# Optimization experiments

Hardware: AMD Instinct MI355X
Metric: run time of the kernel (lower is better)

## Reference

```python
import jax, jax.numpy as jnp
import numpy as np
from jax.ops import segment_sum, segment_max

N, E, F, H, G, P, C = 50000, 600000, 128, 128, 64, 32, 10
HEADS = 3
BN_EPS = 1e-5
COS_EPS = 1e-8


def setup_inputs() -> dict:
    key = jax.random.key(0)
    ks = jax.random.split(key, 32)
    rn = lambda k, shape, s: jax.random.normal(k, shape, jnp.float32) * s
    inp = {
        "x": jax.random.normal(ks[0], (N, F), jnp.float32),
        "edge_index": jax.random.randint(ks[1], (2, E), 0, N, jnp.int32),
        "batch": jnp.sort(jax.random.randint(ks[2], (N,), 0, G, jnp.int32)),
        # GCNConv
        "W1": rn(ks[3], (F, H), F ** -0.5), "b1": jnp.zeros((H,), jnp.float32),
        # SAGEConv (lin_l on aggregated neighbors, lin_r on root)
        "Wl": rn(ks[4], (H, H), H ** -0.5), "Wr": rn(ks[5], (H, H), H ** -0.5),
        "bs": jnp.zeros((H,), jnp.float32),
        # GATConv, heads=3, concat=False
        "Wg": rn(ks[6], (H, HEADS * H), H ** -0.5),
        "a_src": rn(ks[7], (HEADS, H), H ** -0.5),
        "a_dst": rn(ks[8], (HEADS, H), H ** -0.5),
        "bg": jnp.zeros((H,), jnp.float32),
        # prototype head / classifier / decoder
        "protos": jax.random.normal(ks[9], (P, H), jnp.float32),
        "Wc": rn(ks[10], (H, C), H ** -0.5), "bc": jnp.zeros((C,), jnp.float32),
        "Wd1": rn(ks[11], (H, 2 * H), H ** -0.5), "bd1": jnp.zeros((2 * H,), jnp.float32),
        "Wd2": rn(ks[12], (2 * H, F), (2 * H) ** -0.5), "bd2": jnp.zeros((F,), jnp.float32),
    }
    # BatchNorm (eval mode): gamma, beta, running mean/var for bn1..bn3
    for i in range(3):
        k0, k1, k2 = jax.random.split(ks[13 + i], 3)
        inp[f"g{i+1}"] = 1.0 + rn(k0, (H,), 0.05)
        inp[f"be{i+1}"] = rn(k1, (H,), 0.05)
        inp[f"m{i+1}"] = rn(k2, (H,), 0.1)
        inp[f"v{i+1}"] = jnp.ones((H,), jnp.float32)
    return inp


def _bn(x, g, b, m, v):
    return (x - m) * jax.lax.rsqrt(v + BN_EPS) * g + b


def _forward(x, edge_index, batch,
             W1, b1, g1, be1, m1, v1,
             Wl, Wr, bs, g2, be2, m2, v2,
             Wg, a_src, a_dst, bg, g3, be3, m3, v3,
             protos, Wc, bc, Wd1, bd1, Wd2, bd2):
    src, dst = edge_index[0], edge_index[1]
    ones_e = jnp.ones((src.shape[0],), x.dtype)

    # --- GCNConv: symmetric norm with self-loops ---
    h = x @ W1                                        # [N, H]
    deg = segment_sum(ones_e, dst, num_segments=N) + 1.0
    dinv = jax.lax.rsqrt(deg)
    coef = dinv[src] * dinv[dst]                      # [E]
    h1 = segment_sum(h[src] * coef[:, None], dst, num_segments=N)
    h1 = h1 + h * (dinv * dinv)[:, None] + b1         # self-loop term + bias
    h1 = jax.nn.elu(_bn(h1, g1, be1, m1, v1))         # dropout = identity (eval)

    # --- SAGEConv: mean aggregation (no self-loops) ---
    cnt = segment_sum(ones_e, dst, num_segments=N)
    mean_nb = segment_sum(h1[src], dst, num_segments=N) / jnp.maximum(cnt, 1.0)[:, None]
    h2 = mean_nb @ Wl + h1 @ Wr + bs
    h2 = jax.nn.elu(_bn(h2, g2, be2, m2, v2))

    # --- GATConv: heads=3, concat=False (mean), with self-loops ---
    hg = (h2 @ Wg).reshape(N, HEADS, H)               # [N, 3, H]
    al_src = jnp.einsum('nhf,hf->nh', hg, a_src)      # [N, 3]
    al_dst = jnp.einsum('nhf,hf->nh', hg, a_dst)
    loop = jnp.arange(N, dtype=src.dtype)
    s2 = jnp.concatenate([src, loop])
    d2 = jnp.concatenate([dst, loop])
    e = jax.nn.leaky_relu(al_src[s2] + al_dst[d2], 0.2)   # [E+N, 3]
    emax = segment_max(e, d2, num_segments=N)             # every node has a self-loop
    ex = jnp.exp(e - emax[d2])
    den = segment_sum(ex, d2, num_segments=N)
    alpha = ex / den[d2]                                  # [E+N, 3]
    h3 = segment_sum(hg[s2] * alpha[:, :, None], d2, num_segments=N)
    h3 = h3.mean(axis=1) + bg                             # concat=False -> head mean
    h3 = jax.nn.elu(_bn(h3, g3, be3, m3, v3))

    # --- global mean pool over graphs ---
    gcnt = segment_sum(jnp.ones((N,), x.dtype), batch, num_segments=G)
    pooled = segment_sum(h3, batch, num_segments=G) / jnp.maximum(gcnt, 1.0)[:, None]

    # --- prototype head: cosine sim -> softmax -> mix ---
    xn = pooled / jnp.maximum(jnp.linalg.norm(pooled, axis=-1, keepdims=True), COS_EPS)
    pn = protos / jnp.maximum(jnp.linalg.norm(protos, axis=-1, keepdims=True), COS_EPS)
    sims = xn @ pn.T                                      # [G, P]
    assignments = jax.nn.softmax(sims, axis=-1)
    proto_emb = assignments @ protos                      # [G, H]
    logits = proto_emb @ Wc + bc                          # [G, C]
    reconstructed = jax.nn.relu(pooled @ Wd1 + bd1) @ Wd2 + bd2   # [G, F]
    return logits, proto_emb, assignments, reconstructed


def reference(x, edge_index, batch,
              W1, b1, g1, be1, m1, v1,
              Wl, Wr, bs, g2, be2, m2, v2,
              Wg, a_src, a_dst, bg, g3, be3, m3, v3,
              protos, Wc, bc, Wd1, bd1, Wd2, bd2):
    return _forward(x, edge_index, batch,
                    W1, b1, g1, be1, m1, v1,
                    Wl, Wr, bs, g2, be2, m2, v2,
                    Wg, a_src, a_dst, bg, g3, be3, m3, v3,
                    protos, Wc, bc, Wd1, bd1, Wd2, bd2)
```

## Files before the change

### kernel.cpp

```cpp
#include <hip/hip_runtime.h>
#include <hip/hip_bf16.h>
#include <stdint.h>
#include <stddef.h>

#define N_ 50000
#define E_ 600000
#define F_ 128
#define H_ 128
#define G_ 64
#define P_ 32
#define C_ 10
#define NB_ 49

typedef __hip_bfloat16 bf16;
typedef __attribute__((ext_vector_type(8))) short short8;
typedef __attribute__((ext_vector_type(4))) float float4v;

__device__ __forceinline__ float us2f(unsigned short u){ return __uint_as_float(((unsigned int)u)<<16); }
__device__ __forceinline__ unsigned short f2us(float x){ bf16 h = __float2bfloat16(x); return *(unsigned short*)&h; }
__device__ __forceinline__ float blo(unsigned int u){ return __uint_as_float(u<<16); }
__device__ __forceinline__ float bhi(unsigned int u){ return __uint_as_float(u & 0xFFFF0000u); }
__device__ __forceinline__ unsigned int packbf(float lo, float hi){ return ((unsigned int)f2us(hi)<<16) | f2us(lo); }
__device__ __forceinline__ float eluf(float x){ return x>0.f ? x : __expf(x)-1.f; }
__device__ __forceinline__ float bnf(float x,float m,float v,float g,float b){ return (x-m)*rsqrtf(v+1e-5f)*g+b; }
__device__ __forceinline__ float lrelu(float x){ return x>0.f ? x : 0.2f*x; }
__device__ __forceinline__ float expc(float x){ return __expf(fminf(x, 50.f)); }
__device__ __forceinline__ void atomAddF(float* a, float v){ unsafeAtomicAdd(a, v); }

__global__ __launch_bounds__(256) void k_wprep(const float* __restrict__ W1, const float* __restrict__ Wl,
    const float* __restrict__ Wr, const float* __restrict__ Wg, unsigned short* __restrict__ WT){
  int idx = blockIdx.x*256 + threadIdx.x;
  if(idx >= 6*16384) return;
  int m    = idx >> 14;
  int tile = (idx >> 11) & 7;
  int kc   = (idx >> 9) & 3;
  int lane = (idx >> 3) & 63;
  int j    = idx & 7;
  int k = kc*32 + (lane>>4)*8 + j;
  int n = tile*16 + (lane&15);
  float v;
  if(m==0)      v = W1[k*128+n];
  else if(m==1) v = Wl[k*128+n];
  else if(m==2) v = Wr[k*128+n];
  else          v = Wg[k*384 + (m-3)*128 + n];
  WT[idx] = f2us(v);
}

__global__ __launch_bounds__(384) void k_vprep(const float* __restrict__ Wg, const float* __restrict__ a_src,
    const float* __restrict__ a_dst, float* __restrict__ vs3, float* __restrict__ vd3){
  int t = threadIdx.x;
  if(t >= 384) return;
  int h = t >> 7, f = t & 127;
  const float4* wr = (const float4*)(Wg + (size_t)f*384 + h*128);
  const float4* as = (const float4*)(a_src + h*128);
  const float4* ad = (const float4*)(a_dst + h*128);
  float s = 0.f, d = 0.f;
  #pragma unroll 8
  for(int j=0;j<32;j++){
    float4 wv = wr[j], av = as[j], dv = ad[j];
    s += wv.x*av.x + wv.y*av.y + wv.z*av.z + wv.w*av.w;
    d += wv.x*dv.x + wv.y*dv.y + wv.z*dv.z + wv.w*dv.w;
  }
  vs3[t] = s; vd3[t] = d;
}

__device__ __forceinline__ void load_Afrag_bf16(const bf16* A, int row, int lane, short8 af[4]){
  const unsigned short* ap = (const unsigned short*)A + (size_t)row*128 + (lane>>4)*8;
  #pragma unroll
  for(int kc=0;kc<4;kc++) af[kc] = *(const short8*)(ap + kc*32);
}
__device__ __forceinline__ void mfma_pass_g(const unsigned short* __restrict__ WB, const short8 af[4],
                                            int lane, float4v acc[8]){
  #pragma unroll
  for(int tile=0;tile<8;tile++){
    #pragma unroll
    for(int kc=0;kc<4;kc++){
      short8 bfv = *(const short8*)(WB + (((tile*4+kc)*64 + lane)<<3));
      acc[tile] = __builtin_amdgcn_mfma_f32_16x16x32_bf16(af[kc], bfv, acc[tile], 0, 0, 0);
    }
  }
}

__global__ __launch_bounds__(256) void k_mm_x(const float* __restrict__ X, const unsigned short* __restrict__ WTg,
                                              bf16* __restrict__ HB){
// ... 162 lines not shown
                                              int* __restrict__ row_ptr){
  int lane = threadIdx.x;
  int v = (lane < NB_) ? bsum[lane] : 0;
  int x = v;
  #pragma unroll
  for(int o=1;o<64;o<<=1){
    int y = __shfl_up(x, o, 64);
    if(lane >= o) x += y;
  }
  if(lane < NB_) boff[lane] = x - v;
  if(lane == 63) row_ptr[N_] = x;
}

__global__ __launch_bounds__(256) void k_scan3(int* __restrict__ row_ptr, const int* __restrict__ boff,
                                               int* __restrict__ tmp){
  int i = blockIdx.x*256 + threadIdx.x;
  if(i < N_){
    int r = row_ptr[i] + boff[i>>10];
    row_ptr[i] = r;
    tmp[i] = r;
  }
}

__global__ __launch_bounds__(256) void k_scatter(const int* __restrict__ src, const int* __restrict__ dst,
                                                 int* __restrict__ tmp, int* __restrict__ esrc){
  int e = blockIdx.x*256 + threadIdx.x;
  if(e < E_){
    int d = dst[e];
    int pos = atomicAdd(&tmp[d], 1);
    esrc[pos] = src[e];
  }
}

__global__ __launch_bounds__(256) void k_gcn_gather(const int* __restrict__ row_ptr, const int* __restrict__ esrc,
    const float* __restrict__ dinv, const bf16* __restrict__ HB,
    const float* __restrict__ b1, const float* __restrict__ g1, const float* __restrict__ be1,
    const float* __restrict__ m1, const float* __restrict__ v1, bf16* __restrict__ H1B){
  int n = blockIdx.x*4 + (threadIdx.x>>6);
  int lane = threadIdx.x & 63;
  if(n >= N_) return;
  int beg = row_ptr[n], end = row_ptr[n+1];
  float dn = dinv[n];
  float a0 = 0.f, a1 = 0.f;
  const unsigned short* hb = (const unsigned short*)HB;
  int e = beg;
  for(; e+3 < end; e += 4){
    int s0 = esrc[e], s1 = esrc[e+1], s2 = esrc[e+2], s3 = esrc[e+3];
    unsigned int hv0 = *(const unsigned int*)(hb + (size_t)s0*H_ + lane*2);
    unsigned int hv1 = *(const unsigned int*)(hb + (size_t)s1*H_ + lane*2);
    unsigned int hv2 = *(const unsigned int*)(hb + (size_t)s2*H_ + lane*2);
    unsigned int hv3 = *(const unsigned int*)(hb + (size_t)s3*H_ + lane*2);
    float c0 = dinv[s0]*dn, c1 = dinv[s1]*dn, c2 = dinv[s2]*dn, c3 = dinv[s3]*dn;
    a0 += c0*blo(hv0) + c1*blo(hv1) + c2*blo(hv2) + c3*blo(hv3);
    a1 += c0*bhi(hv0) + c1*bhi(hv1) + c2*bhi(hv2) + c3*bhi(hv3);
  }
  for(; e < end; e++){
    int s = esrc[e];
    float c = dinv[s]*dn;
    unsigned int hv = *(const unsigned int*)(hb + (size_t)s*H_ + lane*2);
    a0 += c*blo(hv);
    a1 += c*bhi(hv);
  }
  unsigned int hv = *(const unsigned int*)(hb + (size_t)n*H_ + lane*2);
  int f0 = lane*2, f1 = f0+1;
  float x0 = a0 + blo(hv)*dn*dn + b1[f0];
  float x1 = a1 + bhi(hv)*dn*dn + b1[f1];
  x0 = eluf(bnf(x0, m1[f0], v1[f0], g1[f0], be1[f0]));
  x1 = eluf(bnf(x1, m1[f1], v1[f1], g1[f1], be1[f1]));
  unsigned int o = ((unsigned int)f2us(x1)<<16) | f2us(x0);
  *(unsigned int*)((unsigned short*)H1B + (size_t)n*H_ + lane*2) = o;
}

__global__ __launch_bounds__(256) void k_sage_gather(const int* __restrict__ row_ptr, const int* __restrict__ esrc,
    const bf16* __restrict__ H1B, bf16* __restrict__ MeanB){
  int n = blockIdx.x*4 + (threadIdx.x>>6);
  int lane = threadIdx.x & 63;
  if(n >= N_) return;
  int beg = row_ptr[n], end = row_ptr[n+1];
  float a0 = 0.f, a1 = 0.f;
  const unsigned short* hb = (const unsigned short*)H1B;
  int e = beg;
  for(; e+3 < end; e += 4){
    int s0 = esrc[e], s1 = esrc[e+1], s2 = esrc[e+2], s3 = esrc[e+3];
    unsigned int hv0 = *(const unsigned int*)(hb + (size_t)s0*H_ + lane*2);
    unsigned int hv1 = *(const unsigned int*)(hb + (size_t)s1*H_ + lane*2);
    unsigned int hv2 = *(const unsigned int*)(hb + (size_t)s2*H_ + lane*2);
    unsigned int hv3 = *(const unsigned int*)(hb + (size_t)s3*H_ + lane*2);
    a0 += blo(hv0) + blo(hv1) + blo(hv2) + blo(hv3);
    a1 += bhi(hv0) + bhi(hv1) + bhi(hv2) + bhi(hv3);
  }
  for(; e < end; e++){
    unsigned int hv = *(const unsigned int*)(hb + (size_t)esrc[e]*H_ + lane*2);
    a0 += blo(hv);
    a1 += bhi(hv);
  }
  float inv = 1.f / fmaxf((float)(end-beg), 1.f);
  unsigned int o = ((unsigned int)f2us(a1*inv)<<16) | f2us(a0*inv);
  *(unsigned int*)((unsigned short*)MeanB + (size_t)n*H_ + lane*2) = o;
}

__global__ __launch_bounds__(256) void k_gat_agg(const int* __restrict__ row_ptr, const int* __restrict__ esrc,
    const float* __restrict__ als4, const float* __restrict__ ald4,
    const bf16* __restrict__ H2B, bf16* __restrict__ U){
  int n = blockIdx.x*4 + (threadIdx.x>>6);
  int lane = threadIdx.x & 63;
  if(n >= N_) return;
  int beg = row_ptr[n], end = row_ptr[n+1];
  float4 asn = *(const float4*)(als4 + (size_t)n*4);
  float4 adn = *(const float4*)(ald4 + (size_t)n*4);
  float es0 = expc(lrelu(asn.x + adn.x));
  float es1 = expc(lrelu(asn.y + adn.y));
  float es2 = expc(lrelu(asn.z + adn.z));
  const unsigned short* hb = (const unsigned short*)H2B;
  unsigned int xs = *(const unsigned int*)(hb + (size_t)n*H_ + lane*2);
  float x0 = blo(xs), x1 = bhi(xs);
  float den0 = es0, den1 = es1, den2 = es2;
  float a00 = es0*x0, a01 = es0*x1;
  float a10 = es1*x0, a11 = es1*x1;
  float a20 = es2*x0, a21 = es2*x1;
  for(int c = beg; c < end; c += 64){
    int take = end - c; if(take > 64) take = 64;
    int idx = esrc[c + (lane < take ? lane : take-1)];
    float4 asl = *(const float4*)(als4 + (size_t)idx*4);
    float w0l = expc(lrelu(asl.x + adn.x));
    float w1l = expc(lrelu(asl.y + adn.y));
    float w2l = expc(lrelu(asl.z + adn.z));
    int j = 0;
    for(; j+3 < take; j += 4){
      int s0=__shfl(idx,j),  s1=__shfl(idx,j+1),  s2=__shfl(idx,j+2),  s3=__shfl(idx,j+3);
      float u00=__shfl(w0l,j),   u01=__shfl(w1l,j),   u02=__shfl(w2l,j);
      float u10=__shfl(w0l,j+1), u11=__shfl(w1l,j+1), u12=__shfl(w2l,j+1);
      float u20=__shfl(w0l,j+2), u21=__shfl(w1l,j+2), u22=__shfl(w2l,j+2);
      float u30=__shfl(w0l,j+3), u31=__shfl(w1l,j+3), u32=__shfl(w2l,j+3);
      unsigned int p0 = *(const unsigned int*)(hb + (size_t)s0*H_ + lane*2);
      unsigned int p1 = *(const unsigned int*)(hb + (size_t)s1*H_ + lane*2);
      unsigned int p2 = *(const unsigned int*)(hb + (size_t)s2*H_ + lane*2);
      unsigned int p3 = *(const unsigned int*)(hb + (size_t)s3*H_ + lane*2);
      den0 += u00 + u10 + u20 + u30;
      den1 += u01 + u11 + u21 + u31;
      den2 += u02 + u12 + u22 + u32;
      float q00=blo(p0), q01=bhi(p0), q10=blo(p1), q11=bhi(p1);
      float q20=blo(p2), q21=bhi(p2), q30=blo(p3), q31=bhi(p3);
      a00 += u00*q00 + u10*q10 + u20*q20 + u30*q30;
      a01 += u00*q01 + u10*q11 + u20*q21 + u30*q31;
      a10 += u01*q00 + u11*q10 + u21*q20 + u31*q30;
      a11 += u01*q01 + u11*q11 + u21*q21 + u31*q31;
      a20 += u02*q00 + u12*q10 + u22*q20 + u32*q30;
      a21 += u02*q01 + u12*q11 + u22*q21 + u32*q31;
    }
    for(; j < take; j++){
      int s = __shfl(idx,j);
      float u0=__shfl(w0l,j), u1=__shfl(w1l,j), u2=__shfl(w2l,j);
      unsigned int p = *(const unsigned int*)(hb + (size_t)s*H_ + lane*2);
      float q0 = blo(p), q1 = bhi(p);
      den0 += u0; den1 += u1; den2 += u2;
      a00 += u0*q0; a01 += u0*q1;
      a10 += u1*q0; a11 += u1*q1;
      a20 += u2*q0; a21 += u2*q1;
    }
  }
  float i0 = 1.f/(3.f*den0), i1 = 1.f/(3.f*den1), i2 = 1.f/(3.f*den2);
  unsigned short* ub = (unsigned short*)U;
  size_t ubase = (size_t)n*384 + lane*2;
  *(unsigned int*)(ub + ubase)       = packbf(a00*i0, a01*i0);
  *(unsigned int*)(ub + ubase + 128) = packbf(a10*i1, a11*i1);
  *(unsigned int*)(ub + ubase + 256) = packbf(a20*i2, a21*i2);
}

#define NPW_ 16
__global__ __launch_bounds__(256) void k_h3pool(const bf16* __restrict__ H3B,
    const int* __restrict__ batch, float* __restrict__ pooled, float* __restrict__ gcnt){
  int wave = blockIdx.x*4 + (threadIdx.x>>6);
  int lane = threadIdx.x & 63;
  int n0 = wave*NPW_;
  if(n0 >= N_) return;
  int n1 = n0 + NPW_; if(n1 > N_) n1 = N_;
  int f0 = lane*2, f1 = f0+1;
  float r0=0.f, r1=0.f;
  int cur = batch[n0];
  int seg = 0;
  for(int n=n0; n<n1; n++){
    int b = batch[n];
    if(b != cur){
      atomAddF(&pooled[cur*H_ + f0], r0);
      atomAddF(&pooled[cur*H_ + f1], r1);
      if(lane==0) atomAddF(&gcnt[cur], (float)seg);
      r0 = 0.f; r1 = 0.f; seg = 0; cur = b;
    }
    unsigned int hv = *(const unsigned int*)((const unsigned short*)H3B + (size_t)n*H_ + lane*2);
    r0 += blo(hv);
    r1 += bhi(hv);
    seg++;
  }
  atomAddF(&pooled[cur*H_ + f0], r0);
  atomAddF(&pooled[cur*H_ + f1], r1);
  if(lane==0) atomAddF(&gcnt[cur], (float)seg);
}

__global__ __launch_bounds__(128) void k_head(const float* __restrict__ pooledacc, const float* __restrict__ gcnt,
// ... 71 lines not shown
  const int* src = EI;
  const int* dst = EI + E_;

  int iW1,ib1,iWl,iWr,ibs,iWg,ias,iad,ibg,ipr,iWc,ibc,iWd1,ibd1,iWd2,ibd2;
  int ig1,ibe1,im1,iv1,ig2,ibe2,im2,iv2,ig3,ibe3,im3,iv3;
  if(n_in >= 31 && in_sizes[5] == 128){
    iW1=3; ib1=4; ig1=5; ibe1=6; im1=7; iv1=8;
    iWl=9; iWr=10; ibs=11; ig2=12; ibe2=13; im2=14; iv2=15;
    iWg=16; ias=17; iad=18; ibg=19; ig3=20; ibe3=21; im3=22; iv3=23;
    ipr=24; iWc=25; ibc=26; iWd1=27; ibd1=28; iWd2=29; ibd2=30;
  }else{
    iW1=3; ib1=4; iWl=5; iWr=6; ibs=7; iWg=8; ias=9; iad=10; ibg=11;
    ipr=12; iWc=13; ibc=14; iWd1=15; ibd1=16; iWd2=17; ibd2=18;
    ig1=19; ibe1=20; im1=21; iv1=22; ig2=23; ibe2=24; im2=25; iv2=26;
    ig3=27; ibe3=28; im3=29; iv3=30;
  }
  const float* W1 = (const float*)d_in[iW1];   const float* b1 = (const float*)d_in[ib1];
  const float* Wl = (const float*)d_in[iWl];   const float* Wr = (const float*)d_in[iWr];
  const float* bs = (const float*)d_in[ibs];   const float* Wg = (const float*)d_in[iWg];
  const float* a_src = (const float*)d_in[ias]; const float* a_dst = (const float*)d_in[iad];
  const float* bg = (const float*)d_in[ibg];   const float* protos = (const float*)d_in[ipr];
  const float* Wc = (const float*)d_in[iWc];   const float* bc = (const float*)d_in[ibc];
  const float* Wd1 = (const float*)d_in[iWd1]; const float* bd1 = (const float*)d_in[ibd1];
  const float* Wd2 = (const float*)d_in[iWd2]; const float* bd2 = (const float*)d_in[ibd2];
  const float* g1 = (const float*)d_in[ig1];   const float* be1 = (const float*)d_in[ibe1];
  const float* m1 = (const float*)d_in[im1];   const float* v1 = (const float*)d_in[iv1];
  const float* g2 = (const float*)d_in[ig2];   const float* be2 = (const float*)d_in[ibe2];
  const float* m2 = (const float*)d_in[im2];   const float* v2 = (const float*)d_in[iv2];
  const float* g3 = (const float*)d_in[ig3];   const float* be3 = (const float*)d_in[ibe3];
  const float* m3 = (const float*)d_in[im3];   const float* v3 = (const float*)d_in[iv3];

  const size_t NF = (size_t)N_*H_;
  const size_t intN = (size_t)3*N_ + 4 + (size_t)E_ + 128;
  const size_t fltN = (size_t)9*N_ + G_*H_ + G_ + 768;
  const size_t NEED = NF*2*3 + (size_t)N_*384*2 + intN*4 + fltN*4 + (size_t)6*16384*2;
  if(ws_size < NEED){
    k_sentinel<<<1,1,0,stream>>>((float*)d_out, 1000.f + (float)(ws_size>>20));
    return;
  }
  bf16* RA = (bf16*)d_ws;
  bf16* RB = RA + NF;
  bf16* RC = RB + NF;
  bf16* U  = RC + NF;
  int*  cnt     = (int*)(U + (size_t)N_*384);
  int*  row_ptr = cnt + N_;
  int*  tmp     = row_ptr + (N_+4);
  int*  esrc    = tmp + N_;
  int*  bsum    = esrc + E_;
  int*  boff    = bsum + 64;
  float* dinv   = (float*)(boff + 64);
  float* als4   = dinv + N_;
  float* ald4   = als4 + (size_t)N_*4;
  float* pooled = ald4 + (size_t)N_*4;
  float* gcnt   = pooled + (size_t)G_*H_;
  float* vs3    = gcnt + G_;
  float* vd3    = vs3 + 384;
  unsigned short* WTg = (unsigned short*)(vd3 + 384);

  k_wprep<<<(6*16384+255)/256, 256, 0, stream>>>(W1, Wl, Wr, Wg, WTg);
  k_vprep<<<1, 384, 0, stream>>>(Wg, a_src, a_dst, vs3, vd3);
  hipMemsetAsync(cnt, 0, N_*sizeof(int), stream);
  hipMemsetAsync(pooled, 0, (size_t)(G_*H_+G_)*sizeof(float), stream);
  k_count<<<(E_+255)/256, 256, 0, stream>>>(dst, cnt);
  k_scan1<<<NB_, 1024, 0, stream>>>(cnt, row_ptr, dinv, bsum);
  k_scan2<<<1, 64, 0, stream>>>(bsum, boff, row_ptr);
  k_scan3<<<(N_+255)/256, 256, 0, stream>>>(row_ptr, boff, tmp);
  k_scatter<<<(E_+255)/256, 256, 0, stream>>>(src, dst, tmp, esrc);

  const int GB = (N_+3)/4;
  const int MB = (N_+63)/64;
  k_mm_x<<<MB, 256, 0, stream>>>(X, WTg, RA);
  k_gcn_gather<<<GB, 256, 0, stream>>>(row_ptr, esrc, dinv, RA, b1, g1, be1, m1, v1, RB);
  k_sage_gather<<<GB, 256, 0, stream>>>(row_ptr, esrc, RB, RC);
  k_sage_mm_att<<<MB, 256, 0, stream>>>(RC, RB, WTg + 16384, WTg + 2*16384, bs, g2, be2, m2, v2,
                                        vs3, vd3, RA, als4, ald4);
  k_gat_agg<<<GB, 256, 0, stream>>>(row_ptr, esrc, als4, ald4, RA, U);
  k_gat_mm3<<<MB, 256, 0, stream>>>(U, WTg + 3*16384, bg, g3, be3, m3, v3, RC);
  {
    int waves = (N_ + NPW_ - 1)/NPW_;
    int blocks = (waves + 3)/4;
    k_h3pool<<<blocks, 256, 0, stream>>>(RC, batch, pooled, gcnt);
  }
  k_head<<<G_, 128, 0, stream>>>(pooled, gcnt, protos, Wc, bc, Wd1, bd1, Wd2, bd2, (float*)d_out);
}
```

Measured before the change: 414.5 us.

## Split each wave into four edge groups with 16-byte row loads in gathers

The three neighbor-gather kernels (GCN, SAGE mean, GAT aggregation) now split each 64-lane wave into four groups of 16 lanes. Each group handles a different edge and loads a full 256-byte bf16 row with 16-byte vector loads, and the partial sums are combined with cross-group shuffles at the end. GCN bias plus batch-norm is also folded into a precomputed scale and shift in the prep kernel. This raises memory-level parallelism per wave and cuts instruction count per gathered row. In exchange it needs more accumulator registers, especially in GAT with 24 accumulators, and wastes lanes on the tail edge group.

Measured after the change: 424.1 us. 2.3% more time.

```diff
diff --git a/kernel.cpp b/kernel.cpp
--- a/kernel.cpp
+++ b/kernel.cpp
@@ -16,7 +16,6 @@
 typedef __attribute__((ext_vector_type(8))) short short8;
 typedef __attribute__((ext_vector_type(4))) float float4v;
 
-__device__ __forceinline__ float us2f(unsigned short u){ return __uint_as_float(((unsigned int)u)<<16); }
 __device__ __forceinline__ unsigned short f2us(float x){ bf16 h = __float2bfloat16(x); return *(unsigned short*)&h; }
 __device__ __forceinline__ float blo(unsigned int u){ return __uint_as_float(u<<16); }
 __device__ __forceinline__ float bhi(unsigned int u){ return __uint_as_float(u & 0xFFFF0000u); }
@@ -26,6 +25,11 @@
 __device__ __forceinline__ float lrelu(float x){ return x>0.f ? x : 0.2f*x; }
 __device__ __forceinline__ float expc(float x){ return __expf(fminf(x, 50.f)); }
 __device__ __forceinline__ void atomAddF(float* a, float v){ unsafeAtomicAdd(a, v); }
+__device__ __forceinline__ float xred4(float v){
+  v += __shfl_xor(v, 16, 64);
+  v += __shfl_xor(v, 32, 64);
+  return v;
+}
 
 __global__ __launch_bounds__(256) void k_wprep(const float* __restrict__ W1, const float* __restrict__ Wl,
     const float* __restrict__ Wr, const float* __restrict__ Wg, unsigned short* __restrict__ WT){
@@ -47,9 +51,18 @@
 }
 
 __global__ __launch_bounds__(384) void k_vprep(const float* __restrict__ Wg, const float* __restrict__ a_src,
-    const float* __restrict__ a_dst, float* __restrict__ vs3, float* __restrict__ vd3){
+    const float* __restrict__ a_dst,
+    const float* __restrict__ b1, const float* __restrict__ g1, const float* __restrict__ be1,
+    const float* __restrict__ m1, const float* __restrict__ v1,
+    float* __restrict__ vs3, float* __restrict__ vd3,
+    float* __restrict__ sc1, float* __restrict__ sh1){
   int t = threadIdx.x;
   if(t >= 384) return;
+  if(t < 128){
+    float s = g1[t] * rsqrtf(v1[t] + 1e-5f);
+    sc1[t] = s;
+    sh1[t] = (b1[t] - m1[t]) * s + be1[t];
+  }
   int h = t >> 7, f = t & 127;
   const float4* wr = (const float4*)(Wg + (size_t)f*384 + h*128);
   const float4* as = (const float4*)(a_src + h*128);
@@ -278,43 +291,45 @@
   }
 }
 
+
 __global__ __launch_bounds__(256) void k_gcn_gather(const int* __restrict__ row_ptr, const int* __restrict__ esrc,
     const float* __restrict__ dinv, const bf16* __restrict__ HB,
-    const float* __restrict__ b1, const float* __restrict__ g1, const float* __restrict__ be1,
-    const float* __restrict__ m1, const float* __restrict__ v1, bf16* __restrict__ H1B){
+    const float* __restrict__ sc1, const float* __restrict__ sh1, bf16* __restrict__ H1B){
   int n = blockIdx.x*4 + (threadIdx.x>>6);
   int lane = threadIdx.x & 63;
   if(n >= N_) return;
+  const int g = lane>>4, c = lane&15;
   int beg = row_ptr[n], end = row_ptr[n+1];
   float dn = dinv[n];
-  float a0 = 0.f, a1 = 0.f;
   const unsigned short* hb = (const unsigned short*)HB;
-  int e = beg;
-  for(; e+3 < end; e += 4){
-    int s0 = esrc[e], s1 = esrc[e+1], s2 = esrc[e+2], s3 = esrc[e+3];
-    unsigned int hv0 = *(const unsigned int*)(hb + (size_t)s0*H_ + lane*2);
-    unsigned int hv1 = *(const unsigned int*)(hb + (size_t)s1*H_ + lane*2);
-    unsigned int hv2 = *(const unsigned int*)(hb + (size_t)s2*H_ + lane*2);
-    unsigned int hv3 = *(const unsigned int*)(hb + (size_t)s3*H_ + lane*2);
-    float c0 = dinv[s0]*dn, c1 = dinv[s1]*dn, c2 = dinv[s2]*dn, c3 = dinv[s3]*dn;
-    a0 += c0*blo(hv0) + c1*blo(hv1) + c2*blo(hv2) + c3*blo(hv3);
-    a1 += c0*bhi(hv0) + c1*bhi(hv1) + c2*bhi(hv2) + c3*bhi(hv3);
-  }
-  for(; e < end; e++){
-    int s = esrc[e];
-    float c = dinv[s]*dn;
-    unsigned int hv = *(const unsigned int*)(hb + (size_t)s*H_ + lane*2);
-    a0 += c*blo(hv);
-    a1 += c*bhi(hv);
-  }
-  unsigned int hv = *(const unsigned int*)(hb + (size_t)n*H_ + lane*2);
-  int f0 = lane*2, f1 = f0+1;
-  float x0 = a0 + blo(hv)*dn*dn + b1[f0];
-  float x1 = a1 + bhi(hv)*dn*dn + b1[f1];
-  x0 = eluf(bnf(x0, m1[f0], v1[f0], g1[f0], be1[f0]));
-  x1 = eluf(bnf(x1, m1[f1], v1[f1], g1[f1], be1[f1]));
-  unsigned int o = ((unsigned int)f2us(x1)<<16) | f2us(x0);
-  *(unsigned int*)((unsigned short*)H1B + (size_t)n*H_ + lane*2) = o;
+  uint4 ps = *(const uint4*)(hb + (size_t)n*H_ + c*8);
+  float cw = (g==0) ? dn*dn : 0.f;
+  float a[8];
+  a[0]=cw*blo(ps.x); a[1]=cw*bhi(ps.x); a[2]=cw*blo(ps.y); a[3]=cw*bhi(ps.y);
+  a[4]=cw*blo(ps.z); a[5]=cw*bhi(ps.z); a[6]=cw*blo(ps.w); a[7]=cw*bhi(ps.w);
+  for(int e=beg; e<end; e+=4){
+    int t = end - e;
+    bool act = g < t;
+    int s = esrc[e + (act ? g : 0)];
+    float w = act ? dinv[s]*dn : 0.f;
+    uint4 p = *(const uint4*)(hb + (size_t)s*H_ + c*8);
+    a[0]+=w*blo(p.x); a[1]+=w*bhi(p.x); a[2]+=w*blo(p.y); a[3]+=w*bhi(p.y);
+    a[4]+=w*blo(p.z); a[5]+=w*bhi(p.z); a[6]+=w*blo(p.w); a[7]+=w*bhi(p.w);
+  }
+  #pragma unroll
+  for(int k=0;k<8;k++) a[k] = xred4(a[k]);
+  if(g==0){
+    float4 s0 = *(const float4*)(sc1 + c*8);
+    float4 s1 = *(const float4*)(sc1 + c*8 + 4);
+    float4 t0 = *(const float4*)(sh1 + c*8);
+    float4 t1 = *(const float4*)(sh1 + c*8 + 4);
+    uint4 o;
+    o.x = packbf(eluf(a[0]*s0.x+t0.x), eluf(a[1]*s0.y+t0.y));
+    o.y = packbf(eluf(a[2]*s0.z+t0.z), eluf(a[3]*s0.w+t0.w));
+    o.z = packbf(eluf(a[4]*s1.x+t1.x), eluf(a[5]*s1.y+t1.y));
+    o.w = packbf(eluf(a[6]*s1.z+t1.z), eluf(a[7]*s1.w+t1.w));
+    *(uint4*)((unsigned short*)H1B + (size_t)n*H_ + c*8) = o;
+  }
 }
 
 __global__ __launch_bounds__(256) void k_sage_gather(const int* __restrict__ row_ptr, const int* __restrict__ esrc,
@@ -322,28 +337,43 @@
   int n = blockIdx.x*4 + (threadIdx.x>>6);
   int lane = threadIdx.x & 63;
   if(n >= N_) return;
+  const int g = lane>>4, c = lane&15;
   int beg = row_ptr[n], end = row_ptr[n+1];
-  float a0 = 0.f, a1 = 0.f;
   const unsigned short* hb = (const unsigned short*)H1B;
-  int e = beg;
-  for(; e+3 < end; e += 4){
-    int s0 = esrc[e], s1 = esrc[e+1], s2 = esrc[e+2], s3 = esrc[e+3];
-    unsigned int hv0 = *(const unsigned int*)(hb + (size_t)s0*H_ + lane*2);
-    unsigned int hv1 = *(const unsigned int*)(hb + (size_t)s1*H_ + lane*2);
-    unsigned int hv2 = *(const unsigned int*)(hb + (size_t)s2*H_ + lane*2);
-    unsigned int hv3 = *(const unsigned int*)(hb + (size_t)s3*H_ + lane*2);
-    a0 += blo(hv0) + blo(hv1) + blo(hv2) + blo(hv3);
-    a1 += bhi(hv0) + bhi(hv1) + bhi(hv2) + bhi(hv3);
-  }
-  for(; e < end; e++){
-    unsigned int hv = *(const unsigned int*)(hb + (size_t)esrc[e]*H_ + lane*2);
-    a0 += blo(hv);
-    a1 += bhi(hv);
-  }
-  float inv = 1.f / fmaxf((float)(end-beg), 1.f);
-  unsigned int o = ((unsigned int)f2us(a1*inv)<<16) | f2us(a0*inv);
-  *(unsigned int*)((unsigned short*)MeanB + (size_t)n*H_ + lane*2) = o;
-}
+  float a[8];
+  #pragma unroll
+  for(int k=0;k<8;k++) a[k]=0.f;
+  for(int e=beg; e<end; e+=4){
+    int t = end - e;
+    bool act = g < t;
+    int s = esrc[e + (act ? g : 0)];
+    float w = act ? 1.f : 0.f;
+    uint4 p = *(const uint4*)(hb + (size_t)s*H_ + c*8);
+    a[0]+=w*blo(p.x); a[1]+=w*bhi(p.x); a[2]+=w*blo(p.y); a[3]+=w*bhi(p.y);
+    a[4]+=w*blo(p.z); a[5]+=w*bhi(p.z); a[6]+=w*blo(p.w); a[7]+=w*bhi(p.w);
+  }
+  #pragma unroll
+  for(int k=0;k<8;k++) a[k] = xred4(a[k]);
+  if(g==0){
+    float inv = 1.f / fmaxf((float)(end-beg), 1.f);
+    uint4 o;
+    o.x = packbf(a[0]*inv, a[1]*inv);
+    o.y = packbf(a[2]*inv, a[3]*inv);
+    o.z = packbf(a[4]*inv, a[5]*inv);
+    o.w = packbf(a[6]*inv, a[7]*inv);
+    *(uint4*)((unsigned short*)MeanB + (size_t)n*H_ + c*8) = o;
+  }
+}
+
+#define GAT_STORE8(A, I, OFFH)                                              \
+  {                                                                         \
+    uint4 o;                                                                \
+    o.x = packbf(A[0]*(I), A[1]*(I));                                       \
+    o.y = packbf(A[2]*(I), A[3]*(I));                                       \
+    o.z = packbf(A[4]*(I), A[5]*(I));                                       \
+    o.w = packbf(A[6]*(I), A[7]*(I));                                       \
+    *(uint4*)(ub + (size_t)n*384 + (OFFH)*128 + c*8) = o;                   \
+  }
 
 __global__ __launch_bounds__(256) void k_gat_agg(const int* __restrict__ row_ptr, const int* __restrict__ esrc,
     const float* __restrict__ als4, const float* __restrict__ ald4,
@@ -351,66 +381,52 @@
   int n = blockIdx.x*4 + (threadIdx.x>>6);
   int lane = threadIdx.x & 63;
   if(n >= N_) return;
+  const int g = lane>>4, c = lane&15;
   int beg = row_ptr[n], end = row_ptr[n+1];
+  float4 adn = *(const float4*)(ald4 + (size_t)n*4);
   float4 asn = *(const float4*)(als4 + (size_t)n*4);
-  float4 adn = *(const float4*)(ald4 + (size_t)n*4);
   float es0 = expc(lrelu(asn.x + adn.x));
   float es1 = expc(lrelu(asn.y + adn.y));
   float es2 = expc(lrelu(asn.z + adn.z));
   const unsigned short* hb = (const unsigned short*)H2B;
-  unsigned int xs = *(const unsigned int*)(hb + (size_t)n*H_ + lane*2);
-  float x0 = blo(xs), x1 = bhi(xs);
-  float den0 = es0, den1 = es1, den2 = es2;
-  float a00 = es0*x0, a01 = es0*x1;
-  float a10 = es1*x0, a11 = es1*x1;
-  float a20 = es2*x0, a21 = es2*x1;
-  for(int c = beg; c < end; c += 64){
-    int take = end - c; if(take > 64) take = 64;
-    int idx = esrc[c + (lane < take ? lane : take-1)];
-    float4 asl = *(const float4*)(als4 + (size_t)idx*4);
-    float w0l = expc(lrelu(asl.x + adn.x));
-    float w1l = expc(lrelu(asl.y + adn.y));
-    float w2l = expc(lrelu(asl.z + adn.z));
-    int j = 0;
-    for(; j+3 < take; j += 4){
-      int s0=__shfl(idx,j),  s1=__shfl(idx,j+1),  s2=__shfl(idx,j+2),  s3=__shfl(idx,j+3);
-      float u00=__shfl(w0l,j),   u01=__shfl(w1l,j),   u02=__shfl(w2l,j);
-      float u10=__shfl(w0l,j+1), u11=__shfl(w1l,j+1), u12=__shfl(w2l,j+1);
-      float u20=__shfl(w0l,j+2), u21=__shfl(w1l,j+2), u22=__shfl(w2l,j+2);
-      float u30=__shfl(w0l,j+3), u31=__shfl(w1l,j+3), u32=__shfl(w2l,j+3);
-      unsigned int p0 = *(const unsigned int*)(hb + (size_t)s0*H_ + lane*2);
-      unsigned int p1 = *(const unsigned int*)(hb + (size_t)s1*H_ + lane*2);
-      unsigned int p2 = *(const unsigned int*)(hb + (size_t)s2*H_ + lane*2);
-      unsigned int p3 = *(const unsigned int*)(hb + (size_t)s3*H_ + lane*2);
-      den0 += u00 + u10 + u20 + u30;
-      den1 += u01 + u11 + u21 + u31;
-      den2 += u02 + u12 + u22 + u32;
-      float q00=blo(p0), q01=bhi(p0), q10=blo(p1), q11=bhi(p1);
-      float q20=blo(p2), q21=bhi(p2), q30=blo(p3), q31=bhi(p3);
-      a00 += u00*q00 + u10*q10 + u20*q20 + u30*q30;
-      a01 += u00*q01 + u10*q11 + u20*q21 + u30*q31;
-      a10 += u01*q00 + u11*q10 + u21*q20 + u31*q30;
-      a11 += u01*q01 + u11*q11 + u21*q21 + u31*q31;
-      a20 += u02*q00 + u12*q10 + u22*q20 + u32*q30;
-      a21 += u02*q01 + u12*q11 + u22*q21 + u32*q31;
-    }
-    for(; j < take; j++){
-      int s = __shfl(idx,j);
-      float u0=__shfl(w0l,j), u1=__shfl(w1l,j), u2=__shfl(w2l,j);
-      unsigned int p = *(const unsigned int*)(hb + (size_t)s*H_ + lane*2);
-      float q0 = blo(p), q1 = bhi(p);
-      den0 += u0; den1 += u1; den2 += u2;
-      a00 += u0*q0; a01 += u0*q1;
-      a10 += u1*q0; a11 += u1*q1;
-      a20 += u2*q0; a21 += u2*q1;
-    }
-  }
+  uint4 ps = *(const uint4*)(hb + (size_t)n*H_ + c*8);
+  float w0 = (g==0) ? es0 : 0.f;
+  float w1 = (g==0) ? es1 : 0.f;
+  float w2 = (g==0) ? es2 : 0.f;
+  float f0=blo(ps.x), f1=bhi(ps.x), f2=blo(ps.y), f3=bhi(ps.y);
+  float f4=blo(ps.z), f5=bhi(ps.z), f6=blo(ps.w), f7=bhi(ps.w);
+  float a0[8], a1[8], a2[8];
+  a0[0]=w0*f0; a0[1]=w0*f1; a0[2]=w0*f2; a0[3]=w0*f3; a0[4]=w0*f4; a0[5]=w0*f5; a0[6]=w0*f6; a0[7]=w0*f7;
+  a1[0]=w1*f0; a1[1]=w1*f1; a1[2]=w1*f2; a1[3]=w1*f3; a1[4]=w1*f4; a1[5]=w1*f5; a1[6]=w1*f6; a1[7]=w1*f7;
+  a2[0]=w2*f0; a2[1]=w2*f1; a2[2]=w2*f2; a2[3]=w2*f3; a2[4]=w2*f4; a2[5]=w2*f5; a2[6]=w2*f6; a2[7]=w2*f7;
+  float den0 = w0, den1 = w1, den2 = w2;
+  for(int e=beg; e<end; e+=4){
+    int t = end - e;
+    bool act = g < t;
+    int s = esrc[e + (act ? g : 0)];
+    float4 asl = *(const float4*)(als4 + (size_t)s*4);
+    float u0 = act ? expc(lrelu(asl.x + adn.x)) : 0.f;
+    float u1 = act ? expc(lrelu(asl.y + adn.y)) : 0.f;
+    float u2 = act ? expc(lrelu(asl.z + adn.z)) : 0.f;
+    uint4 p = *(const uint4*)(hb + (size_t)s*H_ + c*8);
+    den0 += u0; den1 += u1; den2 += u2;
+    float q0=blo(p.x), q1=bhi(p.x), q2=blo(p.y), q3=bhi(p.y);
+    float q4=blo(p.z), q5=bhi(p.z), q6=blo(p.w), q7=bhi(p.w);
+    a0[0]+=u0*q0; a0[1]+=u0*q1; a0[2]+=u0*q2; a0[3]+=u0*q3;
+    a0[4]+=u0*q4; a0[5]+=u0*q5; a0[6]+=u0*q6; a0[7]+=u0*q7;
+    a1[0]+=u1*q0; a1[1]+=u1*q1; a1[2]+=u1*q2; a1[3]+=u1*q3;
+    a1[4]+=u1*q4; a1[5]+=u1*q5; a1[6]+=u1*q6; a1[7]+=u1*q7;
+    a2[0]+=u2*q0; a2[1]+=u2*q1; a2[2]+=u2*q2; a2[3]+=u2*q3;
+    a2[4]+=u2*q4; a2[5]+=u2*q5; a2[6]+=u2*q6; a2[7]+=u2*q7;
+  }
+  #pragma unroll
+  for(int k=0;k<8;k++){ a0[k]=xred4(a0[k]); a1[k]=xred4(a1[k]); a2[k]=xred4(a2[k]); }
+  den0 = xred4(den0); den1 = xred4(den1); den2 = xred4(den2);
   float i0 = 1.f/(3.f*den0), i1 = 1.f/(3.f*den1), i2 = 1.f/(3.f*den2);
   unsigned short* ub = (unsigned short*)U;
-  size_t ubase = (size_t)n*384 + lane*2;
-  *(unsigned int*)(ub + ubase)       = packbf(a00*i0, a01*i0);
-  *(unsigned int*)(ub + ubase + 128) = packbf(a10*i1, a11*i1);
-  *(unsigned int*)(ub + ubase + 256) = packbf(a20*i2, a21*i2);
+  if(g==0)      GAT_STORE8(a0, i0, 0)
+  else if(g==1) GAT_STORE8(a1, i1, 1)
+  else if(g==2) GAT_STORE8(a2, i2, 2)
 }
 
 #define NPW_ 16
@@ -548,7 +564,7 @@
 
   const size_t NF = (size_t)N_*H_;
   const size_t intN = (size_t)3*N_ + 4 + (size_t)E_ + 128;
-  const size_t fltN = (size_t)9*N_ + G_*H_ + G_ + 768;
+  const size_t fltN = (size_t)9*N_ + G_*H_ + G_ + 1024;
   const size_t NEED = NF*2*3 + (size_t)N_*384*2 + intN*4 + fltN*4 + (size_t)6*16384*2;
   if(ws_size < NEED){
     k_sentinel<<<1,1,0,stream>>>((float*)d_out, 1000.f + (float)(ws_size>>20));
@@ -571,10 +587,12 @@
   float* gcnt   = pooled + (size_t)G_*H_;
   float* vs3    = gcnt + G_;
   float* vd3    = vs3 + 384;
-  unsigned short* WTg = (unsigned short*)(vd3 + 384);
+  float* sc1    = vd3 + 384;
+  float* sh1    = sc1 + 128;
+  unsigned short* WTg = (unsigned short*)(sh1 + 128);
 
   k_wprep<<<(6*16384+255)/256, 256, 0, stream>>>(W1, Wl, Wr, Wg, WTg);
-  k_vprep<<<1, 384, 0, stream>>>(Wg, a_src, a_dst, vs3, vd3);
+  k_vprep<<<1, 384, 0, stream>>>(Wg, a_src, a_dst, b1, g1, be1, m1, v1, vs3, vd3, sc1, sh1);
   hipMemsetAsync(cnt, 0, N_*sizeof(int), stream);
   hipMemsetAsync(pooled, 0, (size_t)(G_*H_+G_)*sizeof(float), stream);
   k_count<<<(E_+255)/256, 256, 0, stream>>>(dst, cnt);
@@ -586,7 +604,7 @@
   const int GB = (N_+3)/4;
   const int MB = (N_+63)/64;
   k_mm_x<<<MB, 256, 0, stream>>>(X, WTg, RA);
-  k_gcn_gather<<<GB, 256, 0, stream>>>(row_ptr, esrc, dinv, RA, b1, g1, be1, m1, v1, RB);
+  k_gcn_gather<<<GB, 256, 0, stream>>>(row_ptr, esrc, dinv, RA, sc1, sh1, RB);
   k_sage_gather<<<GB, 256, 0, stream>>>(row_ptr, esrc, RB, RC);
   k_sage_mm_att<<<MB, 256, 0, stream>>>(RC, RB, WTg + 16384, WTg + 2*16384, bs, g2, be2, m2, v2,
                                         vs3, vd3, RA, als4, ald4);
```

## Split wave into two half-waves gathering separate edges with 8-byte loads

Applied to the files above, without the earlier changes.

Rewrites the three neighbor-gather kernels (GCN, SAGE, GAT) so each 64-lane wave is split into two 32-lane halves. Each half processes alternate edges, and each lane loads 4 bf16 features with a uint2 load instead of 2 with a uint. Edge indices and weights are loaded cooperatively once per 64-edge chunk and broadcast by shuffle, and the halves are combined with a cross-half xor shuffle at the end. This doubles the edges in flight per wave to improve memory-level parallelism, at the cost of more registers and extra shuffles.

Result: no change. 412.7 us (-0.4%).

```diff
diff --git a/kernel.cpp b/kernel.cpp
--- a/kernel.cpp
+++ b/kernel.cpp
@@ -16,7 +16,6 @@
 typedef __attribute__((ext_vector_type(8))) short short8;
 typedef __attribute__((ext_vector_type(4))) float float4v;
 
-__device__ __forceinline__ float us2f(unsigned short u){ return __uint_as_float(((unsigned int)u)<<16); }
 __device__ __forceinline__ unsigned short f2us(float x){ bf16 h = __float2bfloat16(x); return *(unsigned short*)&h; }
 __device__ __forceinline__ float blo(unsigned int u){ return __uint_as_float(u<<16); }
 __device__ __forceinline__ float bhi(unsigned int u){ return __uint_as_float(u & 0xFFFF0000u); }
@@ -278,6 +277,7 @@
   }
 }
 
+
 __global__ __launch_bounds__(256) void k_gcn_gather(const int* __restrict__ row_ptr, const int* __restrict__ esrc,
     const float* __restrict__ dinv, const bf16* __restrict__ HB,
     const float* __restrict__ b1, const float* __restrict__ g1, const float* __restrict__ be1,
@@ -285,36 +285,57 @@
   int n = blockIdx.x*4 + (threadIdx.x>>6);
   int lane = threadIdx.x & 63;
   if(n >= N_) return;
+  const int g = lane>>5, c = lane&31;
   int beg = row_ptr[n], end = row_ptr[n+1];
   float dn = dinv[n];
-  float a0 = 0.f, a1 = 0.f;
   const unsigned short* hb = (const unsigned short*)HB;
-  int e = beg;
-  for(; e+3 < end; e += 4){
-    int s0 = esrc[e], s1 = esrc[e+1], s2 = esrc[e+2], s3 = esrc[e+3];
-    unsigned int hv0 = *(const unsigned int*)(hb + (size_t)s0*H_ + lane*2);
-    unsigned int hv1 = *(const unsigned int*)(hb + (size_t)s1*H_ + lane*2);
-    unsigned int hv2 = *(const unsigned int*)(hb + (size_t)s2*H_ + lane*2);
-    unsigned int hv3 = *(const unsigned int*)(hb + (size_t)s3*H_ + lane*2);
-    float c0 = dinv[s0]*dn, c1 = dinv[s1]*dn, c2 = dinv[s2]*dn, c3 = dinv[s3]*dn;
-    a0 += c0*blo(hv0) + c1*blo(hv1) + c2*blo(hv2) + c3*blo(hv3);
-    a1 += c0*bhi(hv0) + c1*bhi(hv1) + c2*bhi(hv2) + c3*bhi(hv3);
-  }
-  for(; e < end; e++){
-    int s = esrc[e];
-    float c = dinv[s]*dn;
-    unsigned int hv = *(const unsigned int*)(hb + (size_t)s*H_ + lane*2);
-    a0 += c*blo(hv);
-    a1 += c*bhi(hv);
-  }
-  unsigned int hv = *(const unsigned int*)(hb + (size_t)n*H_ + lane*2);
-  int f0 = lane*2, f1 = f0+1;
-  float x0 = a0 + blo(hv)*dn*dn + b1[f0];
-  float x1 = a1 + bhi(hv)*dn*dn + b1[f1];
-  x0 = eluf(bnf(x0, m1[f0], v1[f0], g1[f0], be1[f0]));
-  x1 = eluf(bnf(x1, m1[f1], v1[f1], g1[f1], be1[f1]));
-  unsigned int o = ((unsigned int)f2us(x1)<<16) | f2us(x0);
-  *(unsigned int*)((unsigned short*)H1B + (size_t)n*H_ + lane*2) = o;
+  uint2 ps = *(const uint2*)(hb + (size_t)n*H_ + c*4);
+  float ws = (g==0) ? dn*dn : 0.f;
+  float a0 = ws*blo(ps.x), a1 = ws*bhi(ps.x), a2 = ws*blo(ps.y), a3 = ws*bhi(ps.y);
+  for(int c0 = beg; c0 < end; c0 += 64){
+    int take = end - c0; if(take > 64) take = 64;
+    int idx = esrc[c0 + (lane < take ? lane : take-1)];
+    float wl = (lane < take) ? dinv[idx]*dn : 0.f;
+    int ro = idx << 7;
+    int j = 0;
+    for(; j+7 < take; j += 8){
+      int e0=j+g, e1=j+2+g, e2=j+4+g, e3=j+6+g;
+      int r0=__shfl(ro,e0), r1=__shfl(ro,e1), r2=__shfl(ro,e2), r3=__shfl(ro,e3);
+      float u0=__shfl(wl,e0), u1=__shfl(wl,e1), u2=__shfl(wl,e2), u3=__shfl(wl,e3);
+      uint2 p0 = *(const uint2*)(hb + r0 + c*4);
+      uint2 p1 = *(const uint2*)(hb + r1 + c*4);
+      uint2 p2 = *(const uint2*)(hb + r2 + c*4);
+      uint2 p3 = *(const uint2*)(hb + r3 + c*4);
+      a0 += u0*blo(p0.x)+u1*blo(p1.x)+u2*blo(p2.x)+u3*blo(p3.x);
+      a1 += u0*bhi(p0.x)+u1*bhi(p1.x)+u2*bhi(p2.x)+u3*bhi(p3.x);
+      a2 += u0*blo(p0.y)+u1*blo(p1.y)+u2*blo(p2.y)+u3*blo(p3.y);
+      a3 += u0*bhi(p0.y)+u1*bhi(p1.y)+u2*bhi(p2.y)+u3*bhi(p3.y);
+    }
+    for(; j < take; j += 2){
+      int e = j + g;
+      int el = e < 64 ? e : 63;
+      int r = __shfl(ro, el);
+      float u = __shfl(wl, el);
+      if(e >= take) u = 0.f;
+      uint2 p = *(const uint2*)(hb + r + c*4);
+      a0 += u*blo(p.x); a1 += u*bhi(p.x); a2 += u*blo(p.y); a3 += u*bhi(p.y);
+    }
+  }
+  a0 += __shfl_xor(a0,32); a1 += __shfl_xor(a1,32);
+  a2 += __shfl_xor(a2,32); a3 += __shfl_xor(a3,32);
+  if(g==0){
+    float4 bv = *(const float4*)(b1 + c*4);
+    float4 mv = *(const float4*)(m1 + c*4);
+    float4 vv = *(const float4*)(v1 + c*4);
+    float4 gv = *(const float4*)(g1 + c*4);
+    float4 ev = *(const float4*)(be1 + c*4);
+    uint2 o;
+    o.x = packbf(eluf(bnf(a0+bv.x, mv.x, vv.x, gv.x, ev.x)),
+                 eluf(bnf(a1+bv.y, mv.y, vv.y, gv.y, ev.y)));
+    o.y = packbf(eluf(bnf(a2+bv.z, mv.z, vv.z, gv.z, ev.z)),
+                 eluf(bnf(a3+bv.w, mv.w, vv.w, gv.w, ev.w)));
+    *(uint2*)((unsigned short*)H1B + (size_t)n*H_ + c*4) = o;
+  }
 }
 
 __global__ __launch_bounds__(256) void k_sage_gather(const int* __restrict__ row_ptr, const int* __restrict__ esrc,
@@ -322,27 +343,48 @@
   int n = blockIdx.x*4 + (threadIdx.x>>6);
   int lane = threadIdx.x & 63;
   if(n >= N_) return;
+  const int g = lane>>5, c = lane&31;
   int beg = row_ptr[n], end = row_ptr[n+1];
-  float a0 = 0.f, a1 = 0.f;
   const unsigned short* hb = (const unsigned short*)H1B;
-  int e = beg;
-  for(; e+3 < end; e += 4){
-    int s0 = esrc[e], s1 = esrc[e+1], s2 = esrc[e+2], s3 = esrc[e+3];
-    unsigned int hv0 = *(const unsigned int*)(hb + (size_t)s0*H_ + lane*2);
-    unsigned int hv1 = *(const unsigned int*)(hb + (size_t)s1*H_ + lane*2);
-    unsigned int hv2 = *(const unsigned int*)(hb + (size_t)s2*H_ + lane*2);
-    unsigned int hv3 = *(const unsigned int*)(hb + (size_t)s3*H_ + lane*2);
-    a0 += blo(hv0) + blo(hv1) + blo(hv2) + blo(hv3);
-    a1 += bhi(hv0) + bhi(hv1) + bhi(hv2) + bhi(hv3);
-  }
-  for(; e < end; e++){
-    unsigned int hv = *(const unsigned int*)(hb + (size_t)esrc[e]*H_ + lane*2);
-    a0 += blo(hv);
-    a1 += bhi(hv);
-  }
-  float inv = 1.f / fmaxf((float)(end-beg), 1.f);
-  unsigned int o = ((unsigned int)f2us(a1*inv)<<16) | f2us(a0*inv);
-  *(unsigned int*)((unsigned short*)MeanB + (size_t)n*H_ + lane*2) = o;
+  float a0=0.f, a1=0.f, a2=0.f, a3=0.f;
+  for(int c0 = beg; c0 < end; c0 += 64){
+    int take = end - c0; if(take > 64) take = 64;
+    int idx = esrc[c0 + (lane < take ? lane : take-1)];
+    float wl = (lane < take) ? 1.f : 0.f;
+    int ro = idx << 7;
+    int j = 0;
+    for(; j+7 < take; j += 8){
+      int e0=j+g, e1=j+2+g, e2=j+4+g, e3=j+6+g;
+      int r0=__shfl(ro,e0), r1=__shfl(ro,e1), r2=__shfl(ro,e2), r3=__shfl(ro,e3);
+      float u0=__shfl(wl,e0), u1=__shfl(wl,e1), u2=__shfl(wl,e2), u3=__shfl(wl,e3);
+      uint2 p0 = *(const uint2*)(hb + r0 + c*4);
+      uint2 p1 = *(const uint2*)(hb + r1 + c*4);
+      uint2 p2 = *(const uint2*)(hb + r2 + c*4);
+      uint2 p3 = *(const uint2*)(hb + r3 + c*4);
+      a0 += u0*blo(p0.x)+u1*blo(p1.x)+u2*blo(p2.x)+u3*blo(p3.x);
+      a1 += u0*bhi(p0.x)+u1*bhi(p1.x)+u2*bhi(p2.x)+u3*bhi(p3.x);
+      a2 += u0*blo(p0.y)+u1*blo(p1.y)+u2*blo(p2.y)+u3*blo(p3.y);
+      a3 += u0*bhi(p0.y)+u1*bhi(p1.y)+u2*bhi(p2.y)+u3*bhi(p3.y);
+    }
+    for(; j < take; j += 2){
+      int e = j + g;
+      int el = e < 64 ? e : 63;
+      int r = __shfl(ro, el);
+      float u = __shfl(wl, el);
+      if(e >= take) u = 0.f;
+      uint2 p = *(const uint2*)(hb + r + c*4);
+      a0 += u*blo(p.x); a1 += u*bhi(p.x); a2 += u*blo(p.y); a3 += u*bhi(p.y);
+    }
+  }
+  a0 += __shfl_xor(a0,32); a1 += __shfl_xor(a1,32);
+  a2 += __shfl_xor(a2,32); a3 += __shfl_xor(a3,32);
+  if(g==0){
+    float inv = 1.f / fmaxf((float)(end-beg), 1.f);
+    uint2 o;
+    o.x = packbf(a0*inv, a1*inv);
+    o.y = packbf(a2*inv, a3*inv);
+    *(uint2*)((unsigned short*)MeanB + (size_t)n*H_ + c*4) = o;
+  }
 }
 
 __global__ __launch_bounds__(256) void k_gat_agg(const int* __restrict__ row_ptr, const int* __restrict__ esrc,
@@ -351,6 +393,7 @@
   int n = blockIdx.x*4 + (threadIdx.x>>6);
   int lane = threadIdx.x & 63;
   if(n >= N_) return;
+  const int g = lane>>5, c = lane&31;
   int beg = row_ptr[n], end = row_ptr[n+1];
   float4 asn = *(const float4*)(als4 + (size_t)n*4);
   float4 adn = *(const float4*)(ald4 + (size_t)n*4);
@@ -358,59 +401,86 @@
   float es1 = expc(lrelu(asn.y + adn.y));
   float es2 = expc(lrelu(asn.z + adn.z));
   const unsigned short* hb = (const unsigned short*)H2B;
-  unsigned int xs = *(const unsigned int*)(hb + (size_t)n*H_ + lane*2);
-  float x0 = blo(xs), x1 = bhi(xs);
-  float den0 = es0, den1 = es1, den2 = es2;
-  float a00 = es0*x0, a01 = es0*x1;
-  float a10 = es1*x0, a11 = es1*x1;
-  float a20 = es2*x0, a21 = es2*x1;
-  for(int c = beg; c < end; c += 64){
-    int take = end - c; if(take > 64) take = 64;
-    int idx = esrc[c + (lane < take ? lane : take-1)];
+  uint2 ps = *(const uint2*)(hb + (size_t)n*H_ + c*4);
+  float w0s = (g==0) ? es0 : 0.f;
+  float w1s = (g==0) ? es1 : 0.f;
+  float w2s = (g==0) ? es2 : 0.f;
+  float f0=blo(ps.x), f1=bhi(ps.x), f2=blo(ps.y), f3=bhi(ps.y);
+  float a00=w0s*f0, a01=w0s*f1, a02=w0s*f2, a03=w0s*f3;
+  float a10=w1s*f0, a11=w1s*f1, a12=w1s*f2, a13=w1s*f3;
+  float a20=w2s*f0, a21=w2s*f1, a22=w2s*f2, a23=w2s*f3;
+  float den0=w0s, den1=w1s, den2=w2s;
+  for(int c0 = beg; c0 < end; c0 += 64){
+    int take = end - c0; if(take > 64) take = 64;
+    int idx = esrc[c0 + (lane < take ? lane : take-1)];
     float4 asl = *(const float4*)(als4 + (size_t)idx*4);
-    float w0l = expc(lrelu(asl.x + adn.x));
-    float w1l = expc(lrelu(asl.y + adn.y));
-    float w2l = expc(lrelu(asl.z + adn.z));
+    bool act = lane < take;
+    float w0l = act ? expc(lrelu(asl.x + adn.x)) : 0.f;
+    float w1l = act ? expc(lrelu(asl.y + adn.y)) : 0.f;
+    float w2l = act ? expc(lrelu(asl.z + adn.z)) : 0.f;
+    int ro = idx << 7;
     int j = 0;
-    for(; j+3 < take; j += 4){
-      int s0=__shfl(idx,j),  s1=__shfl(idx,j+1),  s2=__shfl(idx,j+2),  s3=__shfl(idx,j+3);
-      float u00=__shfl(w0l,j),   u01=__shfl(w1l,j),   u02=__shfl(w2l,j);
-      float u10=__shfl(w0l,j+1), u11=__shfl(w1l,j+1), u12=__shfl(w2l,j+1);
-      float u20=__shfl(w0l,j+2), u21=__shfl(w1l,j+2), u22=__shfl(w2l,j+2);
-      float u30=__shfl(w0l,j+3), u31=__shfl(w1l,j+3), u32=__shfl(w2l,j+3);
-      unsigned int p0 = *(const unsigned int*)(hb + (size_t)s0*H_ + lane*2);
-      unsigned int p1 = *(const unsigned int*)(hb + (size_t)s1*H_ + lane*2);
-      unsigned int p2 = *(const unsigned int*)(hb + (size_t)s2*H_ + lane*2);
-      unsigned int p3 = *(const unsigned int*)(hb + (size_t)s3*H_ + lane*2);
-      den0 += u00 + u10 + u20 + u30;
-      den1 += u01 + u11 + u21 + u31;
-      den2 += u02 + u12 + u22 + u32;
-      float q00=blo(p0), q01=bhi(p0), q10=blo(p1), q11=bhi(p1);
-      float q20=blo(p2), q21=bhi(p2), q30=blo(p3), q31=bhi(p3);
-      a00 += u00*q00 + u10*q10 + u20*q20 + u30*q30;
-      a01 += u00*q01 + u10*q11 + u20*q21 + u30*q31;
-      a10 += u01*q00 + u11*q10 + u21*q20 + u31*q30;
-      a11 += u01*q01 + u11*q11 + u21*q21 + u31*q31;
-      a20 += u02*q00 + u12*q10 + u22*q20 + u32*q30;
-      a21 += u02*q01 + u12*q11 + u22*q21 + u32*q31;
-    }
-    for(; j < take; j++){
-      int s = __shfl(idx,j);
-      float u0=__shfl(w0l,j), u1=__shfl(w1l,j), u2=__shfl(w2l,j);
-      unsigned int p = *(const unsigned int*)(hb + (size_t)s*H_ + lane*2);
-      float q0 = blo(p), q1 = bhi(p);
+    for(; j+7 < take; j += 8){
+      int e0=j+g, e1=j+2+g, e2=j+4+g, e3=j+6+g;
+      int r0=__shfl(ro,e0), r1=__shfl(ro,e1), r2=__shfl(ro,e2), r3=__shfl(ro,e3);
+      float u00=__shfl(w0l,e0), u01=__shfl(w1l,e0), u02=__shfl(w2l,e0);
+      float u10=__shfl(w0l,e1), u11=__shfl(w1l,e1), u12=__shfl(w2l,e1);
+      float u20=__shfl(w0l,e2), u21=__shfl(w1l,e2), u22=__shfl(w2l,e2);
+      float u30=__shfl(w0l,e3), u31=__shfl(w1l,e3), u32=__shfl(w2l,e3);
+      uint2 p0 = *(const uint2*)(hb + r0 + c*4);
+      uint2 p1 = *(const uint2*)(hb + r1 + c*4);
+      uint2 p2 = *(const uint2*)(hb + r2 + c*4);
+      uint2 p3 = *(const uint2*)(hb + r3 + c*4);
+      den0 += u00+u10+u20+u30;
+      den1 += u01+u11+u21+u31;
+      den2 += u02+u12+u22+u32;
+      float q00=blo(p0.x), q01=bhi(p0.x), q02=blo(p0.y), q03=bhi(p0.y);
+      float q10=blo(p1.x), q11=bhi(p1.x), q12=blo(p1.y), q13=bhi(p1.y);
+      float q20=blo(p2.x), q21=bhi(p2.x), q22=blo(p2.y), q23=bhi(p2.y);
+      float q30=blo(p3.x), q31=bhi(p3.x), q32=blo(p3.y), q33=bhi(p3.y);
+      a00 += u00*q00+u10*q10+u20*q20+u30*q30;
+      a01 += u00*q01+u10*q11+u20*q21+u30*q31;
+      a02 += u00*q02+u10*q12+u20*q22+u30*q32;
+      a03 += u00*q03+u10*q13+u20*q23+u30*q33;
+      a10 += u01*q00+u11*q10+u21*q20+u31*q30;
+      a11 += u01*q01+u11*q11+u21*q21+u31*q31;
+      a12 += u01*q02+u11*q12+u21*q22+u31*q32;
+      a13 += u01*q03+u11*q13+u21*q23+u31*q33;
+      a20 += u02*q00+u12*q10+u22*q20+u32*q30;
+      a21 += u02*q01+u12*q11+u22*q21+u32*q31;
+      a22 += u02*q02+u12*q12+u22*q22+u32*q32;
+      a23 += u02*q03+u12*q13+u22*q23+u32*q33;
+    }
+    for(; j < take; j += 2){
+      int e = j + g;
+      int el = e < 64 ? e : 63;
+      int r = __shfl(ro, el);
+      float u0 = __shfl(w0l, el), u1 = __shfl(w1l, el), u2 = __shfl(w2l, el);
+      if(e >= take){ u0 = 0.f; u1 = 0.f; u2 = 0.f; }
+      uint2 p = *(const uint2*)(hb + r + c*4);
+      float q0=blo(p.x), q1=bhi(p.x), q2=blo(p.y), q3=bhi(p.y);
       den0 += u0; den1 += u1; den2 += u2;
-      a00 += u0*q0; a01 += u0*q1;
-      a10 += u1*q0; a11 += u1*q1;
-      a20 += u2*q0; a21 += u2*q1;
-    }
-  }
-  float i0 = 1.f/(3.f*den0), i1 = 1.f/(3.f*den1), i2 = 1.f/(3.f*den2);
-  unsigned short* ub = (unsigned short*)U;
-  size_t ubase = (size_t)n*384 + lane*2;
-  *(unsigned int*)(ub + ubase)       = packbf(a00*i0, a01*i0);
-  *(unsigned int*)(ub + ubase + 128) = packbf(a10*i1, a11*i1);
-  *(unsigned int*)(ub + ubase + 256) = packbf(a20*i2, a21*i2);
+      a00 += u0*q0; a01 += u0*q1; a02 += u0*q2; a03 += u0*q3;
+      a10 += u1*q0; a11 += u1*q1; a12 += u1*q2; a13 += u1*q3;
+      a20 += u2*q0; a21 += u2*q1; a22 += u2*q2; a23 += u2*q3;
+    }
+  }
+  a00 += __shfl_xor(a00,32); a01 += __shfl_xor(a01,32); a02 += __shfl_xor(a02,32); a03 += __shfl_xor(a03,32);
+  a10 += __shfl_xor(a10,32); a11 += __shfl_xor(a11,32); a12 += __shfl_xor(a12,32); a13 += __shfl_xor(a13,32);
+  a20 += __shfl_xor(a20,32); a21 += __shfl_xor(a21,32); a22 += __shfl_xor(a22,32); a23 += __shfl_xor(a23,32);
+  den0 += __shfl_xor(den0,32); den1 += __shfl_xor(den1,32); den2 += __shfl_xor(den2,32);
+  if(g==0){
+    float i0 = 1.f/(3.f*den0), i1 = 1.f/(3.f*den1), i2 = 1.f/(3.f*den2);
+    unsigned short* ub = (unsigned short*)U;
+    size_t ubase = (size_t)n*384 + c*4;
+    uint2 o0, o1, o2;
+    o0.x = packbf(a00*i0, a01*i0); o0.y = packbf(a02*i0, a03*i0);
+    o1.x = packbf(a10*i1, a11*i1); o1.y = packbf(a12*i1, a13*i1);
+    o2.x = packbf(a20*i2, a21*i2); o2.y = packbf(a22*i2, a23*i2);
+    *(uint2*)(ub + ubase)       = o0;
+    *(uint2*)(ub + ubase + 128) = o1;
+    *(uint2*)(ub + ubase + 256) = o2;
+  }
 }
 
 #define NPW_ 16
```
